# Optimization experiments

Hardware: AMD Instinct MI355X
Metric: run time of the kernel (lower is better)

## Reference

```python
import jax, jax.numpy as jnp
import numpy as np

B, M, NV, H, D = 32, 64, 65, 960, 480
ROUNDS = 5
SCALE = D ** -0.5


def _self_att(x, m, qw, qb):
    # x: [B, P, Q, C] attention over Q within each (b, p); m: [B, P, Q]
    qkv = x @ qw.T + qb                      # [B,P,Q,3C]
    q, k, v = jnp.split(qkv, 3, axis=-1)
    # torch builds mask@mask^T/C from a C-times repeated mask == outer product of mask values
    am = m[..., :, None] * m[..., None, :]   # [B,P,Q,Q]
    a = jnp.einsum('bpqc,bpkc->bpqk', q, k) * SCALE
    a = jnp.where(am == 0, -10000.0, a)
    a = jax.nn.softmax(a, axis=-1)
    return jnp.einsum('bpqk,bpkc->bpqc', a, v)


def _attn_logits(x, mask, qw, qb):
    # Attention_logits.forward: attend over value axis, then over key axis
    x = _self_att(x, mask, qw, qb)
    x = _self_att(jnp.swapaxes(x, 1, 2), jnp.swapaxes(mask, 1, 2), qw, qb)
    return jnp.swapaxes(x, 1, 2)


def _biaffine(x1, x2, W, lw, lb):
    # torch.nn.Bilinear (no bias) on the MxN outer grid + Linear(cat(x1,x2)) with bias,
    # computed without materializing the repeated [B,M,N,2D] tensor.
    d = x1.shape[-1]
    bil = jnp.einsum('bmi,oij,bnj->bmno', x1, W, x2)
    lin = (x1 @ lw[:, :d].T)[:, :, None, :] + (x2 @ lw[:, d:].T)[:, None, :, :] + lb
    return bil + lin


def _rounds(key, value, km, vm, W, lw, lb, fw, fb, qw, qb):
    # shared structure of type_classifier / single_classifier (rounds=5, max pooling)
    lm = km[:, :, None] * vm[:, None, :]     # [B,M,N]
    logits = None
    for i in range(ROUNDS):
        logits = _biaffine(key, value, W, lw, lb)          # [B,M,N,out]
        if i < ROUNDS - 1:
            logits = logits @ fw.T + fb                    # [B,M,N,D]
            logits = _attn_logits(logits, lm, qw, qb)
            key = key + logits.max(axis=2)                 # max-pool over values
            value = value + logits.max(axis=1)             # max-pool over keys
        else:
            logits = logits * lm[..., None]
    return logits


def setup_inputs() -> dict:
    root = jax.random.key(0)
    ks = list(jax.random.split(root, 40))
    it = iter(ks)
    nrm = lambda sh, s=0.02: (jax.random.normal(next(it), sh, jnp.float32) * s)
    key = jax.random.normal(next(it), (B, M, H), jnp.float32)
    value = jax.random.normal(next(it), (B, NV, H), jnp.float32)
    klen = jax.random.randint(next(it), (B,), 1, M + 1)
    key_mask = (jnp.arange(M)[None, :] < klen[:, None]).astype(jnp.float32)
    vlen = jax.random.randint(next(it), (B,), 1, NV + 1)
    value_mask = (jnp.arange(NV)[None, :] < vlen[:, None]).astype(jnp.float32)
    return dict(
        key=key, value=value, key_mask=key_mask, value_mask=value_mask,
        w_kt=nrm((D, H)), b_kt=nrm((D,)), w_vt=nrm((D, H)), b_vt=nrm((D,)),
        w_km=nrm((D, H)), b_km=nrm((D,)), w_vm=nrm((D, H)), b_vm=nrm((D,)),
        w_ks=nrm((D, H)), b_ks=nrm((D,)), w_vs=nrm((D, H)), b_vs=nrm((D,)),
        bt_W=nrm((3, D, D)), bt_lw=nrm((3, 2 * D)), bt_lb=nrm((3,)),
        bi_W=nrm((2, D, D)), bi_lw=nrm((2, 2 * D)), bi_lb=nrm((2,)),
        w_ffnt=nrm((D, 3)), b_ffnt=nrm((D,)), w_ffn=nrm((D, 2)), b_ffn=nrm((D,)),
        qkvt_w=nrm((3 * D, D)), qkvt_b=nrm((3 * D,)),
        qkv_w=nrm((3 * D, D)), qkv_b=nrm((3 * D,)),
        w_cls=nrm((2, 2 * D)), b_cls=nrm((2,)),
    )


def reference(key, value, key_mask, value_mask,
              w_kt, b_kt, w_vt, b_vt, w_km, b_km, w_vm, b_vm,
              w_ks, b_ks, w_vs, b_vs,
              bt_W, bt_lw, bt_lb, bi_W, bi_lw, bi_lb,
              w_ffnt, b_ffnt, w_ffn, b_ffn,
              qkvt_w, qkvt_b, qkv_w, qkv_b, w_cls, b_cls):
    # --- type classifier ---
    kt = key @ w_kt.T + b_kt
    vt = value @ w_vt.T + b_vt
    type_logits = _rounds(kt, vt, key_mask, value_mask,
                          bt_W, bt_lw, bt_lb, w_ffnt, b_ffnt, qkvt_w, qkvt_b)  # [B,M,NV,3]
    # drop type token from values
    v1 = value[:, 1:, :]
    vm1 = value_mask[:, 1:]
    type_token = jax.nn.softmax(type_logits[:, :, 0], axis=-1)   # [B,M,3]
    key_type = jnp.argmax(type_token, axis=-1)
    type_single = key_type == 1
    # --- multi classifier (masks unused, as in original) ---
    km_f = key @ w_km.T + b_km
    vm_f = v1 @ w_vm.T + b_vm
    multi_logits = ((km_f @ w_cls[:, :D].T)[:, :, None, :]
                    + (vm_f @ w_cls[:, D:].T)[:, None, :, :] + b_cls)  # [B,M,M? -> B,64,64,2]
    # --- single classifier with key mask restricted to single-link keys ---
    km2 = (key_mask.astype(bool) & type_single).astype(key_mask.dtype)
    ks_f = key @ w_ks.T + b_ks
    vs_f = v1 @ w_vs.T + b_vs
    single_logits = _rounds(ks_f, vs_f, km2, vm1,
                            bi_W, bi_lw, bi_lb, w_ffn, b_ffn, qkv_w, qkv_b)  # [B,64,64,2]
    return (type_logits, multi_logits, single_logits)
```

## Files before the change

### kernel.cpp

```cpp
#include <hip/hip_runtime.h>
#include <math.h>

constexpr int NB = 32;
constexpr int NM = 64;
constexpr int NNV = 65;
constexpr int NH = 960;
constexpr int ND = 480;
constexpr float ATT_SCALE = 0.045643546458763842f;

constexpr int OF_Pq = 0;
constexpr int OF_cq = 4320;
constexpr int OF_Q2 = 5760;
constexpr int OF_V2 = OF_Q2 + 2*1440;
constexpr int OF_dq = 10080;
constexpr int OF_dv = OF_dq + 2*480;
constexpr int OF_S  = 11520;
constexpr int OF_u  = 11529;
constexpr int OF_r  = 11532;
constexpr int OF_w  = 11535;
constexpr int FOLD_SZ = 11552;

typedef float f32x4 __attribute__((ext_vector_type(4)));
typedef short s16x8 __attribute__((ext_vector_type(8)));

__device__ __forceinline__ float wave_sum(float v) {
#pragma unroll
  for (int d = 32; d; d >>= 1) v += __shfl_xor(v, d);
  return v;
}

__device__ __forceinline__ void split_bf16(float x, short& hi, short& lo) {
  union { float f; unsigned u; } a; a.f = x;
  unsigned uh = a.u + 0x7fffu + ((a.u >> 16) & 1u);
  hi = (short)(uh >> 16);
  union { unsigned u; float f; } b; b.u = ((unsigned)(unsigned short)hi) << 16;
  union { float f; unsigned u; } c; c.f = x - b.f;
  unsigned ul = c.u + 0x7fffu + ((c.u >> 16) & 1u);
  lo = (short)(ul >> 16);
}

struct ProjCfg {
  const float* X; const float* W; const float* bias; float* C;
  int R; int x0; int rpb; int xbs;
};
struct Proj6 { ProjCfg c[6]; };

constexpr int KP = 40;

__global__ __launch_bounds__(256) void k_projM(Proj6 P, int K)
{
  __shared__ unsigned short As_hi[64][KP], As_lo[64][KP];
  __shared__ unsigned short Bs_hi[48][KP], Bs_lo[48][KP];
  int p = blockIdx.x, total = gridDim.x;
  int q = total >> 3, r = total & 7;
  int xk = p & 7, idx = p >> 3;
  int lgc = (xk < r) ? (xk * (q + 1) + idx) : (r * (q + 1) + (xk - r) * q + idx);
  int mp = lgc / 10, nx = lgc - mp * 10;
  ProjCfg cfg; int my;
  if      (mp < 32)  { cfg = P.c[0]; my = mp; }
  else if (mp < 65)  { cfg = P.c[1]; my = mp - 32; }
  else if (mp < 97)  { cfg = P.c[2]; my = mp - 65; }
  else if (mp < 129) { cfg = P.c[3]; my = mp - 97; }
  else if (mp < 161) { cfg = P.c[4]; my = mp - 129; }
  else               { cfg = P.c[5]; my = mp - 161; }
  const int m0 = my * 64, n0 = nx * 48;
  const int tid = threadIdx.x;
  const int l6 = tid & 63, w = tid >> 6;
  const int lr = tid >> 2, kc = (tid & 3) * 8;
  const float* Arow = nullptr;
  {
    int rr = m0 + lr;
    if (rr < cfg.R) {
      int b = rr / cfg.rpb, r2 = rr - b * cfg.rpb;
      Arow = cfg.X + (size_t)b * cfg.xbs + (size_t)(cfg.x0 + r2) * K;
    }
  }
  const float* Brow = (lr < 48) ? (cfg.W + (size_t)(n0 + lr) * K) : nullptr;
  const int fr = l6 & 15, fk = (l6 >> 4) * 8;
  f32x4 acc0 = {0.f, 0.f, 0.f, 0.f}, acc1 = acc0, acc2 = acc0;
  for (int k0 = 0; k0 < K; k0 += 32) {
    float xs[8] = {0.f, 0.f, 0.f, 0.f, 0.f, 0.f, 0.f, 0.f};
    if (Arow) {
      float4 a0 = *(const float4*)(Arow + k0 + kc);
      float4 a1 = *(const float4*)(Arow + k0 + kc + 4);
      xs[0] = a0.x; xs[1] = a0.y; xs[2] = a0.z; xs[3] = a0.w;
      xs[4] = a1.x; xs[5] = a1.y; xs[6] = a1.z; xs[7] = a1.w;
    }
    s16x8 vh, vl;
#pragma unroll
    for (int e = 0; e < 8; ++e) { short h, lo2; split_bf16(xs[e], h, lo2); vh[e] = h; vl[e] = lo2; }
    *(s16x8*)&As_hi[lr][kc] = vh;
    *(s16x8*)&As_lo[lr][kc] = vl;
    if (Brow) {
      float4 b0 = *(const float4*)(Brow + k0 + kc);
      float4 b1 = *(const float4*)(Brow + k0 + kc + 4);
      float ys[8] = {b0.x, b0.y, b0.z, b0.w, b1.x, b1.y, b1.z, b1.w};
      s16x8 wh, wl;
#pragma unroll
      for (int e = 0; e < 8; ++e) { short h, lo2; split_bf16(ys[e], h, lo2); wh[e] = h; wl[e] = lo2; }
      *(s16x8*)&Bs_hi[lr][kc] = wh;
      *(s16x8*)&Bs_lo[lr][kc] = wl;
    }
    __syncthreads();
    s16x8 ah = *(const s16x8*)&As_hi[16 * w + fr][fk];
    s16x8 al = *(const s16x8*)&As_lo[16 * w + fr][fk];
    {
      s16x8 bh = *(const s16x8*)&Bs_hi[fr][fk];
      s16x8 bl = *(const s16x8*)&Bs_lo[fr][fk];
      acc0 = __builtin_amdgcn_mfma_f32_16x16x32_bf16(ah, bh, acc0, 0, 0, 0);
      acc0 = __builtin_amdgcn_mfma_f32_16x16x32_bf16(ah, bl, acc0, 0, 0, 0);
      acc0 = __builtin_amdgcn_mfma_f32_16x16x32_bf16(al, bh, acc0, 0, 0, 0);
    }
    {
      s16x8 bh = *(const s16x8*)&Bs_hi[16 + fr][fk];
      s16x8 bl = *(const s16x8*)&Bs_lo[16 + fr][fk];
      acc1 = __builtin_amdgcn_mfma_f32_16x16x32_bf16(ah, bh, acc1, 0, 0, 0);
      acc1 = __builtin_amdgcn_mfma_f32_16x16x32_bf16(ah, bl, acc1, 0, 0, 0);
      acc1 = __builtin_amdgcn_mfma_f32_16x16x32_bf16(al, bh, acc1, 0, 0, 0);
    }
    {
      s16x8 bh = *(const s16x8*)&Bs_hi[32 + fr][fk];
      s16x8 bl = *(const s16x8*)&Bs_lo[32 + fr][fk];
      acc2 = __builtin_amdgcn_mfma_f32_16x16x32_bf16(ah, bh, acc2, 0, 0, 0);
      acc2 = __builtin_amdgcn_mfma_f32_16x16x32_bf16(ah, bl, acc2, 0, 0, 0);
      acc2 = __builtin_amdgcn_mfma_f32_16x16x32_bf16(al, bh, acc2, 0, 0, 0);
    }
    __syncthreads();
  }
#pragma unroll
  for (int c = 0; c < 3; ++c) {
    f32x4 av = (c == 0) ? acc0 : (c == 1) ? acc1 : acc2;
    int n = n0 + 16 * c + fr;
    float bv = cfg.bias[n];
#pragma unroll
    for (int g = 0; g < 4; ++g) {
      int rr = m0 + 16 * w + (l6 >> 4) * 4 + g;
      if (rr < cfg.R) cfg.C[(size_t)rr * ND + n] = av[g] + bv;
    }
  }
}

__global__ __launch_bounds__(256) void k_tmpM(
    const float* __restrict__ Key, const float* __restrict__ W,
    float* __restrict__ T, int O)
{
  __shared__ unsigned short As_hi[64][KP], As_lo[64][KP];
  __shared__ unsigned short Bs_hi[48][KP], Bs_lo[48][KP];
  const int n0 = blockIdx.x * 48;
  const int o = blockIdx.y, b = blockIdx.z;
  const int tid = threadIdx.x;
  const int l6 = tid & 63, w = tid >> 6;
  const int lr = tid >> 2, kc = (tid & 3) * 8;
  const float* Arow = Key + (size_t)b * NM * ND + (size_t)lr * ND;
  const float* Wo = W + (size_t)o * ND * ND;
  const int fr = l6 & 15, fk = (l6 >> 4) * 8;
  f32x4 acc0 = {0.f, 0.f, 0.f, 0.f}, acc1 = acc0, acc2 = acc0;
  for (int k0 = 0; k0 < ND; k0 += 32) {
    {
      float4 a0 = *(const float4*)(Arow + k0 + kc);
      float4 a1 = *(const float4*)(Arow + k0 + kc + 4);
      float xs[8] = {a0.x, a0.y, a0.z, a0.w, a1.x, a1.y, a1.z, a1.w};
      s16x8 vh, vl;
#pragma unroll
      for (int e = 0; e < 8; ++e) { short h, lo2; split_bf16(xs[e], h, lo2); vh[e] = h; vl[e] = lo2; }
      *(s16x8*)&As_hi[lr][kc] = vh;
      *(s16x8*)&As_lo[lr][kc] = vl;
    }
    if (lr < 48) {
      s16x8 wh, wl;
#pragma unroll
      for (int e = 0; e < 8; ++e) {
        float x = Wo[(size_t)(k0 + kc + e) * ND + n0 + lr];
        short h, lo2; split_bf16(x, h, lo2); wh[e] = h; wl[e] = lo2;
      }
      *(s16x8*)&Bs_hi[lr][kc] = wh;
      *(s16x8*)&Bs_lo[lr][kc] = wl;
    }
    __syncthreads();
    s16x8 ah = *(const s16x8*)&As_hi[16 * w + fr][fk];
    s16x8 al = *(const s16x8*)&As_lo[16 * w + fr][fk];
    {
      s16x8 bh = *(const s16x8*)&Bs_hi[fr][fk];
      s16x8 bl = *(const s16x8*)&Bs_lo[fr][fk];
      acc0 = __builtin_amdgcn_mfma_f32_16x16x32_bf16(ah, bh, acc0, 0, 0, 0);
      acc0 = __builtin_amdgcn_mfma_f32_16x16x32_bf16(ah, bl, acc0, 0, 0, 0);
      acc0 = __builtin_amdgcn_mfma_f32_16x16x32_bf16(al, bh, acc0, 0, 0, 0);
    }
    {
      s16x8 bh = *(const s16x8*)&Bs_hi[16 + fr][fk];
      s16x8 bl = *(const s16x8*)&Bs_lo[16 + fr][fk];
      acc1 = __builtin_amdgcn_mfma_f32_16x16x32_bf16(ah, bh, acc1, 0, 0, 0);
      acc1 = __builtin_amdgcn_mfma_f32_16x16x32_bf16(ah, bl, acc1, 0, 0, 0);
      acc1 = __builtin_amdgcn_mfma_f32_16x16x32_bf16(al, bh, acc1, 0, 0, 0);
    }
    {
      s16x8 bh = *(const s16x8*)&Bs_hi[32 + fr][fk];
      s16x8 bl = *(const s16x8*)&Bs_lo[32 + fr][fk];
      acc2 = __builtin_amdgcn_mfma_f32_16x16x32_bf16(ah, bh, acc2, 0, 0, 0);
      acc2 = __builtin_amdgcn_mfma_f32_16x16x32_bf16(ah, bl, acc2, 0, 0, 0);
      acc2 = __builtin_amdgcn_mfma_f32_16x16x32_bf16(al, bh, acc2, 0, 0, 0);
    }
    __syncthreads();
  }
  float* C = T + ((size_t)(b * O + o) * NM) * ND;
#pragma unroll
  for (int c = 0; c < 3; ++c) {
    f32x4 av = (c == 0) ? acc0 : (c == 1) ? acc1 : acc2;
    int n = n0 + 16 * c + fr;
#pragma unroll
    for (int g = 0; g < 4; ++g) {
      int rr = 16 * w + (l6 >> 4) * 4 + g;
      C[(size_t)rr * ND + n] = av[g];
    }
  }
}

template <int O, int NVX>
__global__ __launch_bounds__(256) void k_bilatt0(
    const float* __restrict__ T, const float* __restrict__ Val,
    const float* __restrict__ linK, const float* __restrict__ linV,
    const float* __restrict__ lb, const float* __restrict__ F,
    const float* __restrict__ km, const float* __restrict__ vm,
    int vmOff, int vmStride, float* __restrict__ Y1)
{
  __shared__ float Ls[NVX][3];
  __shared__ float STs[NVX][3];
  __shared__ float hs[NVX], gs[NVX], mkj[NVX];
  __shared__ float Pm[NVX][66];
  __shared__ float rmx[NVX][3];
  __shared__ float rsum[NVX][3];
  __shared__ float ry[NVX][3][3];
  __shared__ float lvs[NVX][3];
  const int b = blockIdx.x >> 6, m = blockIdx.x & 63;
  const int tid = threadIdx.x;
  const int lane = tid & 63, w = tid >> 6;

  for (int j = tid; j < NVX; j += 256) {
    mkj[j] = vm[b * vmStride + vmOff + j];
#pragma unroll
    for (int o = 0; o < O; ++o) lvs[j][o] = linV[((size_t)b * NVX + j) * O + o];
  }
  float4 tsr[O][2];
#pragma unroll
  for (int o = 0; o < O; ++o) {
    const float4* trow = (const float4*)(T + (((size_t)b * O + o) * NM + m) * (size_t)ND);
    tsr[o][0] = trow[lane];
    tsr[o][1] = (lane < 56) ? trow[64 + lane] : make_float4(0.f, 0.f, 0.f, 0.f);
  }
  float lk[O];
#pragma unroll
  for (int o = 0; o < O; ++o) lk[o] = linK[((size_t)b * NM + m) * O + o] + lb[o];
  const float gm = km[b * NM + m];
  const bool gz = (gm == 0.f);

  for (int n = w; n < NVX; n += 4) {
    const float4* vrow = (const float4*)(Val + ((size_t)b * NVX + n) * (size_t)ND);
    float4 v0 = vrow[lane];
    float4 v1 = (lane < 56) ? vrow[64 + lane] : make_float4(0.f, 0.f, 0.f, 0.f);
    float a[3] = {0.f, 0.f, 0.f};
#pragma unroll
    for (int o = 0; o < O; ++o) {
      a[o] = v0.x * tsr[o][0].x + v0.y * tsr[o][0].y + v0.z * tsr[o][0].z + v0.w * tsr[o][0].w
           + v1.x * tsr[o][1].x + v1.y * tsr[o][1].y + v1.z * tsr[o][1].z + v1.w * tsr[o][1].w;
    }
#pragma unroll
    for (int o = 0; o < O; ++o) a[o] = wave_sum(a[o]);
    if (lane == 0) {
#pragma unroll
      for (int o = 0; o < O; ++o) Ls[n][o] = a[o] + lk[o] + lvs[n][o];
      if (O == 2) Ls[n][2] = 0.f;
    }
  }
  __syncthreads();
  const float* Sm = F + OF_S;
  const float u0 = F[OF_u], u1 = F[OF_u + 1], u2 = F[OF_u + 2];
  const float r0 = F[OF_r], r1 = F[OF_r + 1], r2 = F[OF_r + 2];
  const float wc = F[OF_w];
  if (tid < NVX) {
    int j = tid;
    float t0 = Ls[j][0], t1 = Ls[j][1], t2 = Ls[j][2];
    STs[j][0] = t0 * Sm[0] + t1 * Sm[3] + t2 * Sm[6];
    STs[j][1] = t0 * Sm[1] + t1 * Sm[4] + t2 * Sm[7];
    STs[j][2] = t0 * Sm[2] + t1 * Sm[5] + t2 * Sm[8];
    hs[j] = t0 * u0 + t1 * u1 + t2 * u2;
    gs[j] = t0 * r0 + t1 * r1 + t2 * r2;
  }
  __syncthreads();
  const bool act = tid < NVX * 3;
  int i = 0, qq = 0, jlo = 0, jhi = 0;
  float st0 = 0, st1 = 0, st2 = 0, hi = 0;
  bool rowz = true;
  if (act) {
    i = tid / 3; qq = tid - i * 3;
    jlo = qq * 22; jhi = (jlo + 22 < NVX) ? jlo + 22 : NVX;
    st0 = STs[i][0]; st1 = STs[i][1]; st2 = STs[i][2]; hi = hs[i];
    rowz = gz || (mkj[i] == 0.f);
    float mx = -3.0e38f;
    for (int j = jlo; j < jhi; ++j) {
      float s = st0 * Ls[j][0] + st1 * Ls[j][1] + hi + gs[j] + wc;
      if (O == 3) s += st2 * Ls[j][2];
      s = (rowz || mkj[j] == 0.f) ? -10000.f : ATT_SCALE * s;
      Pm[i][j] = s;
      mx = fmaxf(mx, s);
    }
    rmx[i][qq] = mx;
  }
  __syncthreads();
  if (act) {
    float mx = fmaxf(fmaxf(rmx[i][0], rmx[i][1]), rmx[i][2]);
    float sum = 0.f, y0 = 0.f, y1 = 0.f, y2 = 0.f;
    for (int j = jlo; j < jhi; ++j) {
      float pp = __expf(Pm[i][j] - mx);
      sum += pp; y0 += pp * Ls[j][0]; y1 += pp * Ls[j][1];
      if (O == 3) y2 += pp * Ls[j][2];
    }
    rsum[i][qq] = sum; ry[i][qq][0] = y0; ry[i][qq][1] = y1; ry[i][qq][2] = y2;
  }
  __syncthreads();
  if (tid < NVX) {
    int ii = tid;
    float sum = rsum[ii][0] + rsum[ii][1] + rsum[ii][2];
    float y0 = ry[ii][0][0] + ry[ii][1][0] + ry[ii][2][0];
    float y1 = ry[ii][0][1] + ry[ii][1][1] + ry[ii][2][1];
    float y2 = ry[ii][0][2] + ry[ii][1][2] + ry[ii][2][2];
    float inv = 1.f / sum;
    size_t ob = (((size_t)b * NM + m) * NVX + ii) * O;
    Y1[ob + 0] = y0 * inv;
    Y1[ob + 1] = y1 * inv;
    if (O == 3) Y1[ob + 2] = y2 * inv;
  }
}

template <int O, int NVX>
__global__ __launch_bounds__(256) void k_att1vupd(
    const float* __restrict__ Y1, float* __restrict__ Y2,
    const float* __restrict__ F,
    const float* __restrict__ km, const float* __restrict__ vm,
    int vmOff, int vmStride,
    float* __restrict__ valb, const float* __restrict__ lw,
    float* __restrict__ linV)
{
  __shared__ float Ys1[NM][3];
  __shared__ float STs[NM][3];
  __shared__ float hs[NM], gs[NM], mkm[NM];
  __shared__ float Pm[NM][66];
  __shared__ float rmx[NM][3];
  __shared__ float rsum[NM][3];
  __shared__ float ry[NM][3][3];
  __shared__ float Ys2[NM][3];
  __shared__ float vrow[ND];
  const int b = blockIdx.x / NVX, n = blockIdx.x - b * NVX;
  const int tid = threadIdx.x;
  for (int u = tid; u < NM * O; u += 256) {
    int mm = u % NM, o = u / NM;
    Ys1[mm][o] = Y1[(((size_t)b * NM + mm) * NVX + n) * O + o];
  }
  if (tid < NM) {
    mkm[tid] = km[b * NM + tid];
    if (O == 2) Ys1[tid][2] = 0.f;
  }
  const float gm = vm[b * vmStride + vmOff + n];
  const bool gz = (gm == 0.f);
  __syncthreads();
  const float* Sm = F + OF_S + 16;
  const float u0 = F[OF_u + 16], u1 = F[OF_u + 17], u2 = F[OF_u + 18];
  const float r0 = F[OF_r + 16], r1 = F[OF_r + 17], r2 = F[OF_r + 18];
  const float wc = F[OF_w + 16];
  if (tid < NM) {
    int j = tid;
    float t0 = Ys1[j][0], t1 = Ys1[j][1], t2 = Ys1[j][2];
    STs[j][0] = t0 * Sm[0] + t1 * Sm[3] + t2 * Sm[6];
    STs[j][1] = t0 * Sm[1] + t1 * Sm[4] + t2 * Sm[7];
    STs[j][2] = t0 * Sm[2] + t1 * Sm[5] + t2 * Sm[8];
    hs[j] = t0 * u0 + t1 * u1 + t2 * u2;
    gs[j] = t0 * r0 + t1 * r1 + t2 * r2;
  }
  __syncthreads();
  const bool act = tid < NM * 3;
  int i = 0, qq = 0, jlo = 0, jhi = 0;
  float st0 = 0, st1 = 0, st2 = 0, hi = 0;
  bool rowz = true;
  if (act) {
    i = tid / 3; qq = tid - i * 3;
    jlo = qq * 22; jhi = (jlo + 22 < NM) ? jlo + 22 : NM;
    st0 = STs[i][0]; st1 = STs[i][1]; st2 = STs[i][2]; hi = hs[i];
    rowz = gz || (mkm[i] == 0.f);
    float mx = -3.0e38f;
    for (int j = jlo; j < jhi; ++j) {
      float s = st0 * Ys1[j][0] + st1 * Ys1[j][1] + hi + gs[j] + wc;
      if (O == 3) s += st2 * Ys1[j][2];
      s = (rowz || mkm[j] == 0.f) ? -10000.f : ATT_SCALE * s;
      Pm[i][j] = s;
      mx = fmaxf(mx, s);
    }
    rmx[i][qq] = mx;
  }
  __syncthreads();
  if (act) {
    float mx = fmaxf(fmaxf(rmx[i][0], rmx[i][1]), rmx[i][2]);
    float sum = 0.f, y0 = 0.f, y1 = 0.f, y2 = 0.f;
    for (int j = jlo; j < jhi; ++j) {
      float pp = __expf(Pm[i][j] - mx);
      sum += pp; y0 += pp * Ys1[j][0]; y1 += pp * Ys1[j][1];
      if (O == 3) y2 += pp * Ys1[j][2];
    }
    rsum[i][qq] = sum; ry[i][qq][0] = y0; ry[i][qq][1] = y1; ry[i][qq][2] = y2;
  }
  __syncthreads();
  if (tid < NM) {
    int ii = tid;
    float sum = rsum[ii][0] + rsum[ii][1] + rsum[ii][2];
    float y0 = ry[ii][0][0] + ry[ii][1][0] + ry[ii][2][0];
    float y1 = ry[ii][0][1] + ry[ii][1][1] + ry[ii][2][1];
    float y2 = ry[ii][0][2] + ry[ii][1][2] + ry[ii][2][2];
    float inv = 1.f / sum;
    y0 *= inv; y1 *= inv; y2 *= inv;
    size_t ob = (((size_t)b * NVX + n) * NM + ii) * O;
    Y2[ob + 0] = y0; Y2[ob + 1] = y1;
    if (O == 3) Y2[ob + 2] = y2;
    Ys2[ii][0] = y0; Ys2[ii][1] = y1; Ys2[ii][2] = (O == 3) ? y2 : 0.f;
  }
  __syncthreads();
  const float* V2 = F + OF_V2;
  const float* dv = F + OF_dv;
  for (int d = tid; d < ND; d += 256) {
    float v0 = V2[d], v1 = V2[ND + d], v2 = (O == 3) ? V2[2 * ND + d] : 0.f;
    float mx = -3.0e38f;
    for (int j = 0; j < NM; ++j) {
      float s = Ys2[j][0] * v0 + Ys2[j][1] * v1;
      if (O == 3) s += Ys2[j][2] * v2;
      mx = fmaxf(mx, s);
    }
    size_t di = ((size_t)b * NVX + n) * ND + d;
    float nv = valb[di] + mx + dv[d];
    valb[di] = nv;
    vrow[d] = nv;
  }
  __syncthreads();
  const int wv = tid >> 6, lane = tid & 63;
  if (wv < O) {
    float acc = 0.f;
    for (int d = lane; d < ND; d += 64) acc += vrow[d] * lw[(size_t)wv * 2 * ND + ND + d];
    acc = wave_sum(acc);
    if (lane == 0) linV[((size_t)b * NVX + n) * O + wv] = acc;
  }
}

template <int O, int NVX>
__global__ __launch_bounds__(256) void k_kupd(
    const float* __restrict__ Y2, const float* __restrict__ F,
    float* __restrict__ keyb, const float* __restrict__ lw,
    float* __restrict__ linK)
{
  __shared__ float Ys[NVX][3];
  __shared__ float krow[ND];
  const int b = blockIdx.x >> 6, m = blockIdx.x & 63;
  const int tid = threadIdx.x;
  for (int u = tid; u < NVX * O; u += 256) {
    int j = u % NVX, o = u / NVX;
    Ys[j][o] = Y2[(((size_t)b * NVX + j) * NM + m) * O + o];
  }
  __syncthreads();
  const float* V2 = F + OF_V2;
  const float* dv = F + OF_dv;
  for (int d = tid; d < ND; d += 256) {
    float v0 = V2[d], v1 = V2[ND + d], v2 = (O == 3) ? V2[2 * ND + d] : 0.f;
    float mx = -3.0e38f;
    for (int j = 0; j < NVX; ++j) {
      float s = Ys[j][0] * v0 + Ys[j][1] * v1;
      if (O == 3) s += Ys[j][2] * v2;
      mx = fmaxf(mx, s);
    }
    size_t di = ((size_t)b * NM + m) * ND + d;
    float nv = keyb[di] + mx + dv[d];
    keyb[di] = nv;
    krow[d] = nv;
  }
  __syncthreads();
  const int wv = tid >> 6, lane = tid & 63;
  if (wv < O) {
    float acc = 0.f;
    for (int d = lane; d < ND; d += 64) acc += krow[d] * lw[(size_t)wv * 2 * ND + d];
    acc = wave_sum(acc);
    if (lane == 0) linK[((size_t)b * NM + m) * O + wv] = acc;
  }
}

template <int O, int NVX>
__global__ __launch_bounds__(256) void k_bilfin(
    const float* __restrict__ T, const float* __restrict__ Val,
    const float* __restrict__ linK, const float* __restrict__ linV,
    const float* __restrict__ lb, const float* __restrict__ km,
    const float* __restrict__ vm, int vmOff, int vmStride,
    float* __restrict__ Out)
{
  const int b = blockIdx.x >> 6, m = blockIdx.x & 63;
  const int tid = threadIdx.x;
  const int lane = tid & 63, w = tid >> 6;
  float4 tsr[O][2];
#pragma unroll
  for (int o = 0; o < O; ++o) {
    const float4* trow = (const float4*)(T + (((size_t)b * O + o) * NM + m) * (size_t)ND);
    tsr[o][0] = trow[lane];
    tsr[o][1] = (lane < 56) ? trow[64 + lane] : make_float4(0.f, 0.f, 0.f, 0.f);
  }
  float lk[O];
#pragma unroll
  for (int o = 0; o < O; ++o) lk[o] = linK[((size_t)b * NM + m) * O + o] + lb[o];
  const float kmv = km[b * NM + m];
  for (int n = w; n < NVX; n += 4) {
    const float4* vrow = (const float4*)(Val + ((size_t)b * NVX + n) * (size_t)ND);
    float4 v0 = vrow[lane];
    float4 v1 = (lane < 56) ? vrow[64 + lane] : make_float4(0.f, 0.f, 0.f, 0.f);
    float a[3] = {0.f, 0.f, 0.f};
#pragma unroll
    for (int o = 0; o < O; ++o) {
      a[o] = v0.x * tsr[o][0].x + v0.y * tsr[o][0].y + v0.z * tsr[o][0].z + v0.w * tsr[o][0].w
           + v1.x * tsr[o][1].x + v1.y * tsr[o][1].y + v1.z * tsr[o][1].z + v1.w * tsr[o][1].w;
    }
#pragma unroll
    for (int o = 0; o < O; ++o) a[o] = wave_sum(a[o]);
    if (lane == 0) {
      float msk = kmv * vm[b * vmStride + vmOff + n];
      size_t ob = (((size_t)b * NM + m) * NVX + n) * O;
#pragma unroll
      for (int o = 0; o < O; ++o)
        Out[ob + o] = (a[o] + lk[o] + linV[((size_t)b * NVX + n) * O + o]) * msk;
    }
  }
}

struct SpCfg { const float* X; const float* W; float* Out; int R; int O; int wStride; int wOff; };
__global__ __launch_bounds__(256) void k_sproj6(
    SpCfg s0, SpCfg s1, SpCfg s2, SpCfg s3, SpCfg s4, SpCfg s5)
{
  int z = blockIdx.y;
  SpCfg c = (z == 0) ? s0 : (z == 1) ? s1 : (z == 2) ? s2 : (z == 3) ? s3 : (z == 4) ? s4 : s5;
  int gid = blockIdx.x * 4 + (threadIdx.x >> 6);
  if (gid >= c.R * c.O) return;
  int lane = threadIdx.x & 63;
  int r = gid / c.O, o = gid - r * c.O;
  const float* x = c.X + (size_t)r * ND;
  const float* wp = c.W + (size_t)o * c.wStride + c.wOff;
  float acc = 0.f;
  for (int d = lane; d < ND; d += 64) acc += x[d] * wp[d];
  acc = wave_sum(acc);
  if (lane == 0) c.Out[gid] = acc;
}

struct FoldCfg { const float* fw; const float* fb; const float* qw; const float* qb; float* F; int O; };

__global__ __launch_bounds__(256) void k_fold1B(FoldCfg A, FoldCfg Bc)
{
  FoldCfg c = (blockIdx.y == 0) ? A : Bc;
  int O = c.O;
  int gid = blockIdx.x * 4 + (threadIdx.x >> 6);
  int lane = threadIdx.x & 63;
  if (gid >= 3 * ND) return;
  int part = gid / ND, cc0 = gid - part * ND;
  const float* qrow = c.qw + (size_t)(part * ND + cc0) * ND;
  float p0 = 0.f, p1 = 0.f, p2 = 0.f, cc = 0.f;
  for (int d = lane; d < ND; d += 64) {
    float q = qrow[d];
    p0 += c.fw[d * O + 0] * q;
    p1 += c.fw[d * O + 1] * q;
    if (O == 3) p2 += c.fw[d * O + 2] * q;
    cc += c.fb[d] * q;
  }
  p0 = wave_sum(p0); p1 = wave_sum(p1); p2 = wave_sum(p2); cc = wave_sum(cc);
  if (lane == 0) {
    c.F[OF_Pq + part * 1440 + 0 * ND + cc0] = p0;
    c.F[OF_Pq + part * 1440 + 1 * ND + cc0] = p1;
    c.F[OF_Pq + part * 1440 + 2 * ND + cc0] = (O == 3) ? p2 : 0.f;
    c.F[OF_cq + part * ND + cc0] = cc + c.qb[part * ND + cc0];
  }
}

__global__ __launch_bounds__(256) void k_fold2B(FoldCfg A, FoldCfg Bc)
{
  FoldCfg c = (blockIdx.y == 0) ? A : Bc;
  int O = c.O;
  float* F = c.F;
  int gid = blockIdx.x * 4 + (threadIdx.x >> 6);
  int lane = threadIdx.x & 63;
  if (gid < 3 * ND) {
    int part = gid / ND, cc0 = gid - part * ND;
    const float* qrow = c.qw + (size_t)(part * ND + cc0) * ND;
    const float* Pv = F + OF_Pq + 2 * 1440;
    const float* cv = F + OF_cq + 2 * ND;
    float p0 = 0.f, p1 = 0.f, p2 = 0.f, cc = 0.f;
    for (int d = lane; d < ND; d += 64) {
      float q = qrow[d];
      p0 += Pv[0 * ND + d] * q;
      p1 += Pv[1 * ND + d] * q;
      if (O == 3) p2 += Pv[2 * ND + d] * q;
      cc += cv[d] * q;
    }
    p0 = wave_sum(p0); p1 = wave_sum(p1); p2 = wave_sum(p2); cc = wave_sum(cc);
    if (lane == 0) {
      F[OF_Q2 + part * 1440 + 0 * ND + cc0] = p0;
      F[OF_Q2 + part * 1440 + 1 * ND + cc0] = p1;
      F[OF_Q2 + part * 1440 + 2 * ND + cc0] = (O == 3) ? p2 : 0.f;
      F[OF_dq + part * ND + cc0] = cc + c.qb[part * ND + cc0];
    }
  } else if (gid < 3 * ND + 16) {
    int s = gid - 3 * ND;
    const float* Pq = F + OF_Pq;
    const float* Pk = F + OF_Pq + 1440;
    const float* cq = F + OF_cq;
    const float* ck = F + OF_cq + ND;
    float acc = 0.f;
    if (s < 9) {
      int o = s / 3, op = s % 3;
      bool ok = (o < O) && (op < O);
      if (ok) for (int q = lane; q < ND; q += 64) acc += Pq[o * ND + q] * Pk[op * ND + q];
      acc = wave_sum(acc);
      if (lane == 0) F[OF_S + s] = ok ? acc : 0.f;
    } else if (s < 12) {
      int o = s - 9; bool ok = o < O;
      if (ok) for (int q = lane; q < ND; q += 64) acc += Pq[o * ND + q] * ck[q];
      acc = wave_sum(acc);
      if (lane == 0) F[OF_u + o] = ok ? acc : 0.f;
    } else if (s < 15) {
      int o = s - 12; bool ok = o < O;
      if (ok) for (int q = lane; q < ND; q += 64) acc += cq[q] * Pk[o * ND + q];
      acc = wave_sum(acc);
      if (lane == 0) F[OF_r + o] = ok ? acc : 0.f;
    } else {
      for (int q = lane; q < ND; q += 64) acc += cq[q] * ck[q];
      acc = wave_sum(acc);
      if (lane == 0) F[OF_w] = acc;
    }
  }
}

__global__ __launch_bounds__(256) void k_fold3B(FoldCfg A, FoldCfg Bc)
{
  FoldCfg c = (blockIdx.y == 0) ? A : Bc;
  int O = c.O;
  float* F = c.F;
  int s = blockIdx.x * 4 + (threadIdx.x >> 6);
  int lane = threadIdx.x & 63;
  if (s >= 16) return;
  const float* Q2 = F + OF_Q2;
  const float* K2 = F + OF_Q2 + 1440;
  const float* dq = F + OF_dq;
  const float* dk = F + OF_dq + ND;
  float acc = 0.f;
  if (s < 9) {
    int o = s / 3, op = s % 3;
    bool ok = (o < O) && (op < O);
    if (ok) for (int q = lane; q < ND; q += 64) acc += Q2[o * ND + q] * K2[op * ND + q];
    acc = wave_sum(acc);
    if (lane == 0) F[OF_S + 16 + s] = ok ? acc : 0.f;
  } else if (s < 12) {
    int o = s - 9; bool ok = o < O;
    if (ok) for (int q = lane; q < ND; q += 64) acc += Q2[o * ND + q] * dk[q];
    acc = wave_sum(acc);
    if (lane == 0) F[OF_u + 16 + o] = ok ? acc : 0.f;
  } else if (s < 15) {
    int o = s - 12; bool ok = o < O;
    if (ok) for (int q = lane; q < ND; q += 64) acc += dq[q] * K2[o * ND + q];
    acc = wave_sum(acc);
    if (lane == 0) F[OF_r + 16 + o] = ok ? acc : 0.f;
  } else {
    for (int q = lane; q < ND; q += 64) acc += dq[q] * dk[q];
    acc = wave_sum(acc);
    if (lane == 0) F[OF_w + 16] = acc;
  }
}

__global__ void k_type(const float* __restrict__ tl, const float* __restrict__ key_mask,
                       float* __restrict__ km2)
{
  int i = blockIdx.x * blockDim.x + threadIdx.x;
  if (i >= NB * NM) return;
  const float* p = tl + (size_t)i * NNV * 3;
  float l0 = p[0], l1 = p[1], l2 = p[2];
  int arg = 0;
  float best = l0;
  if (l1 > best) { best = l1; arg = 1; }
  if (l2 > best) { best = l2; arg = 2; }
  km2[i] = (key_mask[i] != 0.f && arg == 1) ? 1.f : 0.f;
}

__global__ void k_multi(const float* __restrict__ a, const float* __restrict__ bb,
                        const float* __restrict__ bc, float* __restrict__ out)
{
  int i = blockIdx.x * blockDim.x + threadIdx.x;
  if (i >= NB * NM * NM * 2) return;
  int c = i & 1;
  int t = i >> 1;
  int n = t % NM; t /= NM;
  int m = t % NM;
  int b = t / NM;
  out[i] = a[((size_t)b * NM + m) * 2 + c] + bb[((size_t)b * NM + n) * 2 + c] + bc[c];
}

template <int O, int NVX>
static void run_rounds(hipStream_t stream,
                       float* keyb, float* valb,
                       const float* kmp, const float* vmp, int vmOff, int vmStride,
                       const float* Wb, const float* lwp, const float* lbp,
                       float* fold, float* linK, float* linV,
                       float* tmp, float* Y1, float* Y2, float* outp)
{
  dim3 blk(256);
  for (int r = 0; r < 5; ++r) {
    k_tmpM<<<dim3(10, O, NB), blk, 0, stream>>>(keyb, Wb, tmp, O);
    if (r < 4) {
      k_bilatt0<O, NVX><<<dim3(NB * NM), blk, 0, stream>>>(
          tmp, valb, linK, linV, lbp, fold, kmp, vmp, vmOff, vmStride, Y1);
      k_att1vupd<O, NVX><<<dim3(NB * NVX), blk, 0, stream>>>(
          Y1, Y2, fold, kmp, vmp, vmOff, vmStride, valb, lwp, linV);
      k_kupd<O, NVX><<<dim3(NB * NM), blk, 0, stream>>>(Y2, fold, keyb, lwp, linK);
    } else {
      k_bilfin<O, NVX><<<dim3(NB * NM), blk, 0, stream>>>(
          tmp, valb, linK, linV, lbp, kmp, vmp, vmOff, vmStride, outp);
    }
  }
}

extern "C" void kernel_launch(void* const* d_in, const int* in_sizes, int n_in,
                              void* d_out, int out_size, void* d_ws, size_t ws_size,
                              hipStream_t stream)
{
  const float* key        = (const float*)d_in[0];
  const float* value      = (const float*)d_in[1];
  const float* key_mask   = (const float*)d_in[2];
  const float* value_mask = (const float*)d_in[3];
  const float* w_kt = (const float*)d_in[4];  const float* b_kt = (const float*)d_in[5];
  const float* w_vt = (const float*)d_in[6];  const float* b_vt = (const float*)d_in[7];
  const float* w_km = (const float*)d_in[8];  const float* b_km = (const float*)d_in[9];
  const float* w_vm = (const float*)d_in[10]; const float* b_vm = (const float*)d_in[11];
  const float* w_ks = (const float*)d_in[12]; const float* b_ks = (const float*)d_in[13];
  const float* w_vs = (const float*)d_in[14]; const float* b_vs = (const float*)d_in[15];
  const float* bt_W = (const float*)d_in[16]; const float* bt_lw = (const float*)d_in[17];
  const float* bt_lb = (const float*)d_in[18];
  const float* bi_W = (const float*)d_in[19]; const float* bi_lw = (const float*)d_in[20];
  const float* bi_lb = (const float*)d_in[21];
  const float* w_ffnt = (const float*)d_in[22]; const float* b_ffnt = (const float*)d_in[23];
  const float* w_ffn  = (const float*)d_in[24]; const float* b_ffn  = (const float*)d_in[25];
  const float* qkvt_w = (const float*)d_in[26]; const float* qkvt_b = (const float*)d_in[27];
  const float* qkv_w  = (const float*)d_in[28]; const float* qkv_b  = (const float*)d_in[29];
  const float* w_cls  = (const float*)d_in[30]; const float* b_cls  = (const float*)d_in[31];

  float* ws = (float*)d_ws;
  size_t off = 0;
  float* kt_t  = ws + off; off += (size_t)NB * NM * ND;
  float* vt_t  = ws + off; off += (size_t)NB * NNV * ND;
  float* kt_s  = ws + off; off += (size_t)NB * NM * ND;
  float* vt_s  = ws + off; off += (size_t)NB * NM * ND;
  float* tmp   = ws + off; off += (size_t)NB * 3 * NM * ND;
  float* Y1    = ws + off; off += (size_t)NB * NM * NNV * 3;
  float* Y2    = ws + off; off += (size_t)NB * NM * NNV * 3;
  float* linK_t = ws + off; off += (size_t)NB * NM * 3;
  float* linV_t = ws + off; off += (size_t)NB * NNV * 3;
  float* linK_s = ws + off; off += (size_t)NB * NM * 3;
  float* linV_s = ws + off; off += (size_t)NB * NM * 3;
  float* fold_t = ws + off; off += FOLD_SZ;
  float* fold_s = ws + off; off += FOLD_SZ;
  float* km2   = ws + off; off += (size_t)NB * NM;
  float* a2    = ws + off; off += (size_t)NB * NM * 2;
  float* b2    = ws + off; off += (size_t)NB * NM * 2;
  (void)off; (void)ws_size; (void)in_sizes; (void)n_in; (void)out_size;

  float* kmf = tmp;
  float* vmf = tmp + (size_t)NB * NM * ND;

  float* out_type   = (float*)d_out;
  float* out_multi  = out_type + (size_t)NB * NM * NNV * 3;
  float* out_single = out_multi + (size_t)NB * NM * NM * 2;

  dim3 blk(256);

  Proj6 P;
  P.c[0] = { key,   w_kt, b_kt, kt_t, NB * NM,  0, NM,  NM * NH };
  P.c[1] = { value, w_vt, b_vt, vt_t, NB * NNV, 0, NNV, NNV * NH };
  P.c[2] = { key,   w_ks, b_ks, kt_s, NB * NM,  0, NM,  NM * NH };
  P.c[3] = { value, w_vs, b_vs, vt_s, NB * NM,  1, NM,  NNV * NH };
  P.c[4] = { key,   w_km, b_km, kmf,  NB * NM,  0, NM,  NM * NH };
  P.c[5] = { value, w_vm, b_vm, vmf,  NB * NM,  1, NM,  NNV * NH };
  k_projM<<<dim3(193 * 10), blk, 0, stream>>>(P, NH);

  FoldCfg ft = { w_ffnt, b_ffnt, qkvt_w, qkvt_b, fold_t, 3 };
  FoldCfg fs = { w_ffn,  b_ffn,  qkv_w,  qkv_b,  fold_s, 2 };
  k_fold1B<<<dim3(360, 2), blk, 0, stream>>>(ft, fs);
  k_fold2B<<<dim3(364, 2), blk, 0, stream>>>(ft, fs);
  k_fold3B<<<dim3(4, 2), blk, 0, stream>>>(ft, fs);

  SpCfg s0 = { kt_t, bt_lw, linK_t, NB * NM,  3, 2 * ND, 0 };
  SpCfg s1 = { vt_t, bt_lw, linV_t, NB * NNV, 3, 2 * ND, ND };
  SpCfg s2 = { kt_s, bi_lw, linK_s, NB * NM,  2, 2 * ND, 0 };
  SpCfg s3 = { vt_s, bi_lw, linV_s, NB * NM,  2, 2 * ND, ND };
  SpCfg s4 = { kmf,  w_cls, a2,     NB * NM,  2, 2 * ND, 0 };
  SpCfg s5 = { vmf,  w_cls, b2,     NB * NM,  2, 2 * ND, ND };
  k_sproj6<<<dim3((NB * NNV * 3 + 3) / 4, 6), blk, 0, stream>>>(s0, s1, s2, s3, s4, s5);

  k_multi<<<dim3((NB * NM * NM * 2 + 255) / 256), blk, 0, stream>>>(a2, b2, b_cls, out_multi);

  run_rounds<3, NNV>(stream, kt_t, vt_t, key_mask, value_mask, 0, NNV,
                     bt_W, bt_lw, bt_lb, fold_t, linK_t, linV_t,
                     tmp, Y1, Y2, out_type);

  k_type<<<dim3(8), blk, 0, stream>>>(out_type, key_mask, km2);

  run_rounds<2, NM>(stream, kt_s, vt_s, km2, value_mask, 1, NNV,
                    bi_W, bi_lw, bi_lb, fold_s, linK_s, linV_s,
                    tmp, Y1, Y2, out_single);
}
```

Before: 1.097 ms.

## Fuse all biaffine-attention rounds into one persistent per-batch mega kernel

Replaces the per-round sequence of bilinear, attention and key/value update kernels with a single 1024-thread kernel per batch that loops over all five rounds. Bilinear weights are pre-transposed and split into bf16 hi/lo once, and key/value states are kept as bf16 hi/lo pairs updated in place, with logits held in shared memory. This removes dozens of launches and global round-trips of intermediate tensors. The cost is only 32 blocks across the GPU, leaving most compute units idle.

```diff
diff --git a/kernel.cpp b/kernel.cpp
--- a/kernel.cpp
+++ b/kernel.cpp
@@ -20,6 +20,7 @@
 constexpr int OF_w  = 11535;
 constexpr int FOLD_SZ = 11552;
 
+typedef unsigned short u16;
 typedef float f32x4 __attribute__((ext_vector_type(4)));
 typedef short s16x8 __attribute__((ext_vector_type(8)));
 
@@ -39,8 +40,39 @@
   lo = (short)(ul >> 16);
 }
 
+__device__ __forceinline__ float join_bf16(u16 h, u16 l) {
+  union { unsigned u; float f; } a, b;
+  a.u = ((unsigned)h) << 16; b.u = ((unsigned)l) << 16;
+  return a.f + b.f;
+}
+
+__global__ __launch_bounds__(256) void k_cvtT(
+    const float* __restrict__ btW, const float* __restrict__ biW,
+    u16* __restrict__ wtHi, u16* __restrict__ wtLo)
+{
+  __shared__ float s[32][33];
+  const int z = blockIdx.z;
+  const float* src = (z < 3) ? (btW + (size_t)z * ND * ND) : (biW + (size_t)(z - 3) * ND * ND);
+  u16* dh = wtHi + (size_t)z * ND * ND;
+  u16* dl = wtLo + (size_t)z * ND * ND;
+  const int k0 = blockIdx.y * 32, n0 = blockIdx.x * 32;
+  const int tx = threadIdx.x & 31, ty = threadIdx.x >> 5;
+#pragma unroll
+  for (int q = 0; q < 4; ++q)
+    s[ty + q * 8][tx] = src[(size_t)(k0 + ty + q * 8) * ND + n0 + tx];
+  __syncthreads();
+#pragma unroll
+  for (int q = 0; q < 4; ++q) {
+    float v = s[tx][ty + q * 8];
+    short h, l; split_bf16(v, h, l);
+    size_t di = (size_t)(n0 + ty + q * 8) * ND + k0 + tx;
+    dh[di] = (u16)h; dl[di] = (u16)l;
+  }
+}
+
 struct ProjCfg {
   const float* X; const float* W; const float* bias; float* C;
+  u16* pH; u16* pL;
   int R; int x0; int rpb; int xbs;
 };
 struct Proj6 { ProjCfg c[6]; };
@@ -49,8 +81,8 @@
 
 __global__ __launch_bounds__(256) void k_projM(Proj6 P, int K)
 {
-  __shared__ unsigned short As_hi[64][KP], As_lo[64][KP];
-  __shared__ unsigned short Bs_hi[48][KP], Bs_lo[48][KP];
+  __shared__ u16 As_hi[64][KP], As_lo[64][KP];
+  __shared__ u16 Bs_hi[48][KP], Bs_lo[48][KP];
   int p = blockIdx.x, total = gridDim.x;
   int q = total >> 3, r = total & 7;
   int xk = p & 7, idx = p >> 3;
@@ -135,397 +167,263 @@
 #pragma unroll
     for (int g = 0; g < 4; ++g) {
       int rr = m0 + 16 * w + (l6 >> 4) * 4 + g;
-      if (rr < cfg.R) cfg.C[(size_t)rr * ND + n] = av[g] + bv;
-    }
-  }
-}
-
-__global__ __launch_bounds__(256) void k_tmpM(
-    const float* __restrict__ Key, const float* __restrict__ W,
-    float* __restrict__ T, int O)
-{
-  __shared__ unsigned short As_hi[64][KP], As_lo[64][KP];
-  __shared__ unsigned short Bs_hi[48][KP], Bs_lo[48][KP];
-  const int n0 = blockIdx.x * 48;
-  const int o = blockIdx.y, b = blockIdx.z;
+      if (rr < cfg.R) {
+        float v = av[g] + bv;
+        size_t di = (size_t)rr * ND + n;
+        cfg.C[di] = v;
+        if (cfg.pH) {
+          short h, lo2; split_bf16(v, h, lo2);
+          cfg.pH[di] = (u16)h; cfg.pL[di] = (u16)lo2;
+        }
+      }
+    }
+  }
+}
+
+template <int O, int NVX>
+__global__ __launch_bounds__(1024, 4) void k_mega(
+    const u16* __restrict__ WtH, const u16* __restrict__ WtL,
+    u16* __restrict__ tmpH, u16* __restrict__ tmpL,
+    u16* __restrict__ keyH, u16* __restrict__ keyL,
+    u16* __restrict__ valH, u16* __restrict__ valL,
+    const float* __restrict__ kmp, const float* __restrict__ vmp, int vmOff, int vmStride,
+    const float* __restrict__ F, const float* __restrict__ lw, const float* __restrict__ lb,
+    const float* __restrict__ linK0, const float* __restrict__ linV0,
+    float* __restrict__ outp)
+{
+  constexpr int NT = (NVX + 15) >> 4;
+  __shared__ float Lb[NM][NVX][3];
+  __shared__ float Yb[NM][NVX][3];
+  __shared__ float linKL[NM][3];
+  __shared__ float linVL[NVX][3];
+  __shared__ float kmL[NM];
+  __shared__ float vmL[NVX];
+  const int b = blockIdx.x;
   const int tid = threadIdx.x;
-  const int l6 = tid & 63, w = tid >> 6;
-  const int lr = tid >> 2, kc = (tid & 3) * 8;
-  const float* Arow = Key + (size_t)b * NM * ND + (size_t)lr * ND;
-  const float* Wo = W + (size_t)o * ND * ND;
-  const int fr = l6 & 15, fk = (l6 >> 4) * 8;
-  f32x4 acc0 = {0.f, 0.f, 0.f, 0.f}, acc1 = acc0, acc2 = acc0;
-  for (int k0 = 0; k0 < ND; k0 += 32) {
+  const int w = tid >> 6, l = tid & 63;
+  const int fr = l & 15, fko = (l >> 4) * 8;
+  const int rquad = (l >> 4) * 4;
+
+  if (tid < NM) {
+    kmL[tid] = kmp[b * NM + tid];
+#pragma unroll
+    for (int o = 0; o < O; ++o) linKL[tid][o] = linK0[(size_t)(b * NM + tid) * O + o];
+  } else if (tid >= 128 && tid - 128 < NVX) {
+    int n = tid - 128;
+    vmL[n] = vmp[b * vmStride + vmOff + n];
+#pragma unroll
+    for (int o = 0; o < O; ++o) linVL[n][o] = linV0[(size_t)(b * NVX + n) * O + o];
+  }
+  float SmA[9], SmB[9];
+#pragma unroll
+  for (int s = 0; s < 9; ++s) { SmA[s] = F[OF_S + s]; SmB[s] = F[OF_S + 16 + s]; }
+  float uA[3], uB[3], rA[3], rB[3];
+#pragma unroll
+  for (int s = 0; s < 3; ++s) {
+    uA[s] = F[OF_u + s]; uB[s] = F[OF_u + 16 + s];
+    rA[s] = F[OF_r + s]; rB[s] = F[OF_r + 16 + s];
+  }
+  const float wA = F[OF_w], wB = F[OF_w + 16];
+  const float* V2 = F + OF_V2;
+  const float* dvp = F + OF_dv;
+
+  const size_t bK = (size_t)b * NM * ND;
+  const size_t bV = (size_t)b * NVX * ND;
+  u16* tH = tmpH + (size_t)b * O * NM * ND;
+  u16* tL = tmpL + (size_t)b * O * NM * ND;
+  const u16* kHb = keyH + bK; const u16* kLb = keyL + bK;
+  const u16* vHb = valH + bV; const u16* vLb = valL + bV;
+  const s16x8 zf = {0, 0, 0, 0, 0, 0, 0, 0};
+
+  for (int r = 0; r < 5; ++r) {
+    __syncthreads();
     {
-      float4 a0 = *(const float4*)(Arow + k0 + kc);
-      float4 a1 = *(const float4*)(Arow + k0 + kc + 4);
-      float xs[8] = {a0.x, a0.y, a0.z, a0.w, a1.x, a1.y, a1.z, a1.w};
-      s16x8 vh, vl;
-#pragma unroll
-      for (int e = 0; e < 8; ++e) { short h, lo2; split_bf16(xs[e], h, lo2); vh[e] = h; vl[e] = lo2; }
-      *(s16x8*)&As_hi[lr][kc] = vh;
-      *(s16x8*)&As_lo[lr][kc] = vl;
-    }
-    if (lr < 48) {
-      s16x8 wh, wl;
-#pragma unroll
-      for (int e = 0; e < 8; ++e) {
-        float x = Wo[(size_t)(k0 + kc + e) * ND + n0 + lr];
-        short h, lo2; split_bf16(x, h, lo2); wh[e] = h; wl[e] = lo2;
+      const int GJ = O * 30;
+      for (int t = w; t < GJ; t += 16) {
+        int o = t / 30, nt = t - o * 30;
+        const u16* bH = WtH + ((size_t)o * ND + nt * 16 + fr) * ND + fko;
+        const u16* bL2 = WtL + ((size_t)o * ND + nt * 16 + fr) * ND + fko;
+        f32x4 z4 = {0.f, 0.f, 0.f, 0.f};
+        f32x4 am[4] = {z4, z4, z4, z4};
+#pragma unroll 3
+        for (int k0 = 0; k0 < ND; k0 += 32) {
+          s16x8 bh = *(const s16x8*)(bH + k0);
+          s16x8 bl = *(const s16x8*)(bL2 + k0);
+#pragma unroll
+          for (int mt = 0; mt < 4; ++mt) {
+            s16x8 ah = *(const s16x8*)(kHb + (size_t)(mt * 16 + fr) * ND + fko + k0);
+            s16x8 al = *(const s16x8*)(kLb + (size_t)(mt * 16 + fr) * ND + fko + k0);
+            am[mt] = __builtin_amdgcn_mfma_f32_16x16x32_bf16(ah, bh, am[mt], 0, 0, 0);
+            am[mt] = __builtin_amdgcn_mfma_f32_16x16x32_bf16(ah, bl, am[mt], 0, 0, 0);
+            am[mt] = __builtin_amdgcn_mfma_f32_16x16x32_bf16(al, bh, am[mt], 0, 0, 0);
+          }
+        }
+        int n = nt * 16 + fr;
+#pragma unroll
+        for (int mt = 0; mt < 4; ++mt)
+#pragma unroll
+          for (int g = 0; g < 4; ++g) {
+            int m = mt * 16 + rquad + g;
+            short h, lo2; split_bf16(am[mt][g], h, lo2);
+            size_t di = ((size_t)o * NM + m) * ND + n;
+            tH[di] = (u16)h; tL[di] = (u16)lo2;
+          }
       }
-      *(s16x8*)&Bs_hi[lr][kc] = wh;
-      *(s16x8*)&Bs_lo[lr][kc] = wl;
     }
     __syncthreads();
-    s16x8 ah = *(const s16x8*)&As_hi[16 * w + fr][fk];
-    s16x8 al = *(const s16x8*)&As_lo[16 * w + fr][fk];
+    const bool finalr = (r == 4);
     {
-      s16x8 bh = *(const s16x8*)&Bs_hi[fr][fk];
-      s16x8 bl = *(const s16x8*)&Bs_lo[fr][fk];
-      acc0 = __builtin_amdgcn_mfma_f32_16x16x32_bf16(ah, bh, acc0, 0, 0, 0);
-      acc0 = __builtin_amdgcn_mfma_f32_16x16x32_bf16(ah, bl, acc0, 0, 0, 0);
-      acc0 = __builtin_amdgcn_mfma_f32_16x16x32_bf16(al, bh, acc0, 0, 0, 0);
-    }
-    {
-      s16x8 bh = *(const s16x8*)&Bs_hi[16 + fr][fk];
-      s16x8 bl = *(const s16x8*)&Bs_lo[16 + fr][fk];
-      acc1 = __builtin_amdgcn_mfma_f32_16x16x32_bf16(ah, bh, acc1, 0, 0, 0);
-      acc1 = __builtin_amdgcn_mfma_f32_16x16x32_bf16(ah, bl, acc1, 0, 0, 0);
-      acc1 = __builtin_amdgcn_mfma_f32_16x16x32_bf16(al, bh, acc1, 0, 0, 0);
-    }
-    {
-      s16x8 bh = *(const s16x8*)&Bs_hi[32 + fr][fk];
-      s16x8 bl = *(const s16x8*)&Bs_lo[32 + fr][fk];
-      acc2 = __builtin_amdgcn_mfma_f32_16x16x32_bf16(ah, bh, acc2, 0, 0, 0);
-      acc2 = __builtin_amdgcn_mfma_f32_16x16x32_bf16(ah, bl, acc2, 0, 0, 0);
-      acc2 = __builtin_amdgcn_mfma_f32_16x16x32_bf16(al, bh, acc2, 0, 0, 0);
-    }
+      const int BJ = O * NT;
+      for (int t = w; t < BJ; t += 16) {
+        int o = t / NT, nt = t - o * NT;
+        int n = nt * 16 + fr;
+        bool nok = n < NVX;
+        const u16* bH = vHb + (size_t)(nok ? n : 0) * ND + fko;
+        const u16* bL2 = vLb + (size_t)(nok ? n : 0) * ND + fko;
+        f32x4 z4 = {0.f, 0.f, 0.f, 0.f};
+        f32x4 am[4] = {z4, z4, z4, z4};
+#pragma unroll 3
+        for (int k0 = 0; k0 < ND; k0 += 32) {
+          s16x8 bh = nok ? *(const s16x8*)(bH + k0) : zf;
+          s16x8 bl = nok ? *(const s16x8*)(bL2 + k0) : zf;
+#pragma unroll
+          for (int mt = 0; mt < 4; ++mt) {
+            s16x8 ah = *(const s16x8*)(tH + ((size_t)o * NM + mt * 16 + fr) * ND + fko + k0);
+            s16x8 al = *(const s16x8*)(tL + ((size_t)o * NM + mt * 16 + fr) * ND + fko + k0);
+            am[mt] = __builtin_amdgcn_mfma_f32_16x16x32_bf16(ah, bh, am[mt], 0, 0, 0);
+            am[mt] = __builtin_amdgcn_mfma_f32_16x16x32_bf16(ah, bl, am[mt], 0, 0, 0);
+            am[mt] = __builtin_amdgcn_mfma_f32_16x16x32_bf16(al, bh, am[mt], 0, 0, 0);
+          }
+        }
+        if (nok) {
+          float lbo = lb[o];
+#pragma unroll
+          for (int mt = 0; mt < 4; ++mt)
+#pragma unroll
+            for (int g = 0; g < 4; ++g) {
+              int m = mt * 16 + rquad + g;
+              float v = am[mt][g] + linKL[m][o] + linVL[n][o] + lbo;
+              if (!finalr) Lb[m][n][o] = v;
+              else outp[(((size_t)b * NM + m) * NVX + n) * O + o] = v * kmL[m] * vmL[n];
+            }
+        }
+      }
+    }
+    if (finalr) break;
     __syncthreads();
-  }
-  float* C = T + ((size_t)(b * O + o) * NM) * ND;
-#pragma unroll
-  for (int c = 0; c < 3; ++c) {
-    f32x4 av = (c == 0) ? acc0 : (c == 1) ? acc1 : acc2;
-    int n = n0 + 16 * c + fr;
-#pragma unroll
-    for (int g = 0; g < 4; ++g) {
-      int rr = 16 * w + (l6 >> 4) * 4 + g;
-      C[(size_t)rr * ND + n] = av[g];
-    }
-  }
-}
-
-template <int O, int NVX>
-__global__ __launch_bounds__(256) void k_bilatt0(
-    const float* __restrict__ T, const float* __restrict__ Val,
-    const float* __restrict__ linK, const float* __restrict__ linV,
-    const float* __restrict__ lb, const float* __restrict__ F,
-    const float* __restrict__ km, const float* __restrict__ vm,
-    int vmOff, int vmStride, float* __restrict__ Y1)
-{
-  __shared__ float Ls[NVX][3];
-  __shared__ float STs[NVX][3];
-  __shared__ float hs[NVX], gs[NVX], mkj[NVX];
-  __shared__ float Pm[NVX][66];
-  __shared__ float rmx[NVX][3];
-  __shared__ float rsum[NVX][3];
-  __shared__ float ry[NVX][3][3];
-  __shared__ float lvs[NVX][3];
-  const int b = blockIdx.x >> 6, m = blockIdx.x & 63;
-  const int tid = threadIdx.x;
-  const int lane = tid & 63, w = tid >> 6;
-
-  for (int j = tid; j < NVX; j += 256) {
-    mkj[j] = vm[b * vmStride + vmOff + j];
-#pragma unroll
-    for (int o = 0; o < O; ++o) lvs[j][o] = linV[((size_t)b * NVX + j) * O + o];
-  }
-  float4 tsr[O][2];
-#pragma unroll
-  for (int o = 0; o < O; ++o) {
-    const float4* trow = (const float4*)(T + (((size_t)b * O + o) * NM + m) * (size_t)ND);
-    tsr[o][0] = trow[lane];
-    tsr[o][1] = (lane < 56) ? trow[64 + lane] : make_float4(0.f, 0.f, 0.f, 0.f);
-  }
-  float lk[O];
-#pragma unroll
-  for (int o = 0; o < O; ++o) lk[o] = linK[((size_t)b * NM + m) * O + o] + lb[o];
-  const float gm = km[b * NM + m];
-  const bool gz = (gm == 0.f);
-
-  for (int n = w; n < NVX; n += 4) {
-    const float4* vrow = (const float4*)(Val + ((size_t)b * NVX + n) * (size_t)ND);
-    float4 v0 = vrow[lane];
-    float4 v1 = (lane < 56) ? vrow[64 + lane] : make_float4(0.f, 0.f, 0.f, 0.f);
-    float a[3] = {0.f, 0.f, 0.f};
-#pragma unroll
-    for (int o = 0; o < O; ++o) {
-      a[o] = v0.x * tsr[o][0].x + v0.y * tsr[o][0].y + v0.z * tsr[o][0].z + v0.w * tsr[o][0].w
-           + v1.x * tsr[o][1].x + v1.y * tsr[o][1].y + v1.z * tsr[o][1].z + v1.w * tsr[o][1].w;
-    }
-#pragma unroll
-    for (int o = 0; o < O; ++o) a[o] = wave_sum(a[o]);
-    if (lane == 0) {
-#pragma unroll
-      for (int o = 0; o < O; ++o) Ls[n][o] = a[o] + lk[o] + lvs[n][o];
-      if (O == 2) Ls[n][2] = 0.f;
-    }
-  }
-  __syncthreads();
-  const float* Sm = F + OF_S;
-  const float u0 = F[OF_u], u1 = F[OF_u + 1], u2 = F[OF_u + 2];
-  const float r0 = F[OF_r], r1 = F[OF_r + 1], r2 = F[OF_r + 2];
-  const float wc = F[OF_w];
-  if (tid < NVX) {
-    int j = tid;
-    float t0 = Ls[j][0], t1 = Ls[j][1], t2 = Ls[j][2];
-    STs[j][0] = t0 * Sm[0] + t1 * Sm[3] + t2 * Sm[6];
-    STs[j][1] = t0 * Sm[1] + t1 * Sm[4] + t2 * Sm[7];
-    STs[j][2] = t0 * Sm[2] + t1 * Sm[5] + t2 * Sm[8];
-    hs[j] = t0 * u0 + t1 * u1 + t2 * u2;
-    gs[j] = t0 * r0 + t1 * r1 + t2 * r2;
-  }
-  __syncthreads();
-  const bool act = tid < NVX * 3;
-  int i = 0, qq = 0, jlo = 0, jhi = 0;
-  float st0 = 0, st1 = 0, st2 = 0, hi = 0;
-  bool rowz = true;
-  if (act) {
-    i = tid / 3; qq = tid - i * 3;
-    jlo = qq * 22; jhi = (jlo + 22 < NVX) ? jlo + 22 : NVX;
-    st0 = STs[i][0]; st1 = STs[i][1]; st2 = STs[i][2]; hi = hs[i];
-    rowz = gz || (mkj[i] == 0.f);
-    float mx = -3.0e38f;
-    for (int j = jlo; j < jhi; ++j) {
-      float s = st0 * Ls[j][0] + st1 * Ls[j][1] + hi + gs[j] + wc;
-      if (O == 3) s += st2 * Ls[j][2];
-      s = (rowz || mkj[j] == 0.f) ? -10000.f : ATT_SCALE * s;
-      Pm[i][j] = s;
-      mx = fmaxf(mx, s);
-    }
-    rmx[i][qq] = mx;
-  }
-  __syncthreads();
-  if (act) {
-    float mx = fmaxf(fmaxf(rmx[i][0], rmx[i][1]), rmx[i][2]);
-    float sum = 0.f, y0 = 0.f, y1 = 0.f, y2 = 0.f;
-    for (int j = jlo; j < jhi; ++j) {
-      float pp = __expf(Pm[i][j] - mx);
-      sum += pp; y0 += pp * Ls[j][0]; y1 += pp * Ls[j][1];
-      if (O == 3) y2 += pp * Ls[j][2];
-    }
-    rsum[i][qq] = sum; ry[i][qq][0] = y0; ry[i][qq][1] = y1; ry[i][qq][2] = y2;
-  }
-  __syncthreads();
-  if (tid < NVX) {
-    int ii = tid;
-    float sum = rsum[ii][0] + rsum[ii][1] + rsum[ii][2];
-    float y0 = ry[ii][0][0] + ry[ii][1][0] + ry[ii][2][0];
-    float y1 = ry[ii][0][1] + ry[ii][1][1] + ry[ii][2][1];
-    float y2 = ry[ii][0][2] + ry[ii][1][2] + ry[ii][2][2];
-    float inv = 1.f / sum;
-    size_t ob = (((size_t)b * NM + m) * NVX + ii) * O;
-    Y1[ob + 0] = y0 * inv;
-    Y1[ob + 1] = y1 * inv;
-    if (O == 3) Y1[ob + 2] = y2 * inv;
-  }
-}
-
-template <int O, int NVX>
-__global__ __launch_bounds__(256) void k_att1vupd(
-    const float* __restrict__ Y1, float* __restrict__ Y2,
-    const float* __restrict__ F,
-    const float* __restrict__ km, const float* __restrict__ vm,
-    int vmOff, int vmStride,
-    float* __restrict__ valb, const float* __restrict__ lw,
-    float* __restrict__ linV)
-{
-  __shared__ float Ys1[NM][3];
-  __shared__ float STs[NM][3];
-  __shared__ float hs[NM], gs[NM], mkm[NM];
-  __shared__ float Pm[NM][66];
-  __shared__ float rmx[NM][3];
-  __shared__ float rsum[NM][3];
-  __shared__ float ry[NM][3][3];
-  __shared__ float Ys2[NM][3];
-  __shared__ float vrow[ND];
-  const int b = blockIdx.x / NVX, n = blockIdx.x - b * NVX;
-  const int tid = threadIdx.x;
-  for (int u = tid; u < NM * O; u += 256) {
-    int mm = u % NM, o = u / NM;
-    Ys1[mm][o] = Y1[(((size_t)b * NM + mm) * NVX + n) * O + o];
-  }
-  if (tid < NM) {
-    mkm[tid] = km[b * NM + tid];
-    if (O == 2) Ys1[tid][2] = 0.f;
-  }
-  const float gm = vm[b * vmStride + vmOff + n];
-  const bool gz = (gm == 0.f);
-  __syncthreads();
-  const float* Sm = F + OF_S + 16;
-  const float u0 = F[OF_u + 16], u1 = F[OF_u + 17], u2 = F[OF_u + 18];
-  const float r0 = F[OF_r + 16], r1 = F[OF_r + 17], r2 = F[OF_r + 18];
-  const float wc = F[OF_w + 16];
-  if (tid < NM) {
-    int j = tid;
-    float t0 = Ys1[j][0], t1 = Ys1[j][1], t2 = Ys1[j][2];
-    STs[j][0] = t0 * Sm[0] + t1 * Sm[3] + t2 * Sm[6];
-    STs[j][1] = t0 * Sm[1] + t1 * Sm[4] + t2 * Sm[7];
-    STs[j][2] = t0 * Sm[2] + t1 * Sm[5] + t2 * Sm[8];
-    hs[j] = t0 * u0 + t1 * u1 + t2 * u2;
-    gs[j] = t0 * r0 + t1 * r1 + t2 * r2;
-  }
-  __syncthreads();
-  const bool act = tid < NM * 3;
-  int i = 0, qq = 0, jlo = 0, jhi = 0;
-  float st0 = 0, st1 = 0, st2 = 0, hi = 0;
-  bool rowz = true;
-  if (act) {
-    i = tid / 3; qq = tid - i * 3;
-    jlo = qq * 22; jhi = (jlo + 22 < NM) ? jlo + 22 : NM;
-    st0 = STs[i][0]; st1 = STs[i][1]; st2 = STs[i][2]; hi = hs[i];
-    rowz = gz || (mkm[i] == 0.f);
-    float mx = -3.0e38f;
-    for (int j = jlo; j < jhi; ++j) {
-      float s = st0 * Ys1[j][0] + st1 * Ys1[j][1] + hi + gs[j] + wc;
-      if (O == 3) s += st2 * Ys1[j][2];
-      s = (rowz || mkm[j] == 0.f) ? -10000.f : ATT_SCALE * s;
-      Pm[i][j] = s;
-      mx = fmaxf(mx, s);
-    }
-    rmx[i][qq] = mx;
-  }
-  __syncthreads();
-  if (act) {
-    float mx = fmaxf(fmaxf(rmx[i][0], rmx[i][1]), rmx[i][2]);
-    float sum = 0.f, y0 = 0.f, y1 = 0.f, y2 = 0.f;
-    for (int j = jlo; j < jhi; ++j) {
-      float pp = __expf(Pm[i][j] - mx);
-      sum += pp; y0 += pp * Ys1[j][0]; y1 += pp * Ys1[j][1];
-      if (O == 3) y2 += pp * Ys1[j][2];
-    }
-    rsum[i][qq] = sum; ry[i][qq][0] = y0; ry[i][qq][1] = y1; ry[i][qq][2] = y2;
-  }
-  __syncthreads();
-  if (tid < NM) {
-    int ii = tid;
-    float sum = rsum[ii][0] + rsum[ii][1] + rsum[ii][2];
-    float y0 = ry[ii][0][0] + ry[ii][1][0] + ry[ii][2][0];
-    float y1 = ry[ii][0][1] + ry[ii][1][1] + ry[ii][2][1];
-    float y2 = ry[ii][0][2] + ry[ii][1][2] + ry[ii][2][2];
-    float inv = 1.f / sum;
-    y0 *= inv; y1 *= inv; y2 *= inv;
-    size_t ob = (((size_t)b * NVX + n) * NM + ii) * O;
-    Y2[ob + 0] = y0; Y2[ob + 1] = y1;
-    if (O == 3) Y2[ob + 2] = y2;
-    Ys2[ii][0] = y0; Ys2[ii][1] = y1; Ys2[ii][2] = (O == 3) ? y2 : 0.f;
-  }
-  __syncthreads();
-  const float* V2 = F + OF_V2;
-  const float* dv = F + OF_dv;
-  for (int d = tid; d < ND; d += 256) {
-    float v0 = V2[d], v1 = V2[ND + d], v2 = (O == 3) ? V2[2 * ND + d] : 0.f;
-    float mx = -3.0e38f;
-    for (int j = 0; j < NM; ++j) {
-      float s = Ys2[j][0] * v0 + Ys2[j][1] * v1;
-      if (O == 3) s += Ys2[j][2] * v2;
-      mx = fmaxf(mx, s);
-    }
-    size_t di = ((size_t)b * NVX + n) * ND + d;
-    float nv = valb[di] + mx + dv[d];
-    valb[di] = nv;
-    vrow[d] = nv;
-  }
-  __syncthreads();
-  const int wv = tid >> 6, lane = tid & 63;
-  if (wv < O) {
-    float acc = 0.f;
-    for (int d = lane; d < ND; d += 64) acc += vrow[d] * lw[(size_t)wv * 2 * ND + ND + d];
-    acc = wave_sum(acc);
-    if (lane == 0) linV[((size_t)b * NVX + n) * O + wv] = acc;
-  }
-}
-
-template <int O, int NVX>
-__global__ __launch_bounds__(256) void k_kupd(
-    const float* __restrict__ Y2, const float* __restrict__ F,
-    float* __restrict__ keyb, const float* __restrict__ lw,
-    float* __restrict__ linK)
-{
-  __shared__ float Ys[NVX][3];
-  __shared__ float krow[ND];
-  const int b = blockIdx.x >> 6, m = blockIdx.x & 63;
-  const int tid = threadIdx.x;
-  for (int u = tid; u < NVX * O; u += 256) {
-    int j = u % NVX, o = u / NVX;
-    Ys[j][o] = Y2[(((size_t)b * NVX + j) * NM + m) * O + o];
-  }
-  __syncthreads();
-  const float* V2 = F + OF_V2;
-  const float* dv = F + OF_dv;
-  for (int d = tid; d < ND; d += 256) {
-    float v0 = V2[d], v1 = V2[ND + d], v2 = (O == 3) ? V2[2 * ND + d] : 0.f;
-    float mx = -3.0e38f;
-    for (int j = 0; j < NVX; ++j) {
-      float s = Ys[j][0] * v0 + Ys[j][1] * v1;
-      if (O == 3) s += Ys[j][2] * v2;
-      mx = fmaxf(mx, s);
-    }
-    size_t di = ((size_t)b * NM + m) * ND + d;
-    float nv = keyb[di] + mx + dv[d];
-    keyb[di] = nv;
-    krow[d] = nv;
-  }
-  __syncthreads();
-  const int wv = tid >> 6, lane = tid & 63;
-  if (wv < O) {
-    float acc = 0.f;
-    for (int d = lane; d < ND; d += 64) acc += krow[d] * lw[(size_t)wv * 2 * ND + d];
-    acc = wave_sum(acc);
-    if (lane == 0) linK[((size_t)b * NM + m) * O + wv] = acc;
-  }
-}
-
-template <int O, int NVX>
-__global__ __launch_bounds__(256) void k_bilfin(
-    const float* __restrict__ T, const float* __restrict__ Val,
-    const float* __restrict__ linK, const float* __restrict__ linV,
-    const float* __restrict__ lb, const float* __restrict__ km,
-    const float* __restrict__ vm, int vmOff, int vmStride,
-    float* __restrict__ Out)
-{
-  const int b = blockIdx.x >> 6, m = blockIdx.x & 63;
-  const int tid = threadIdx.x;
-  const int lane = tid & 63, w = tid >> 6;
-  float4 tsr[O][2];
-#pragma unroll
-  for (int o = 0; o < O; ++o) {
-    const float4* trow = (const float4*)(T + (((size_t)b * O + o) * NM + m) * (size_t)ND);
-    tsr[o][0] = trow[lane];
-    tsr[o][1] = (lane < 56) ? trow[64 + lane] : make_float4(0.f, 0.f, 0.f, 0.f);
-  }
-  float lk[O];
-#pragma unroll
-  for (int o = 0; o < O; ++o) lk[o] = linK[((size_t)b * NM + m) * O + o] + lb[o];
-  const float kmv = km[b * NM + m];
-  for (int n = w; n < NVX; n += 4) {
-    const float4* vrow = (const float4*)(Val + ((size_t)b * NVX + n) * (size_t)ND);
-    float4 v0 = vrow[lane];
-    float4 v1 = (lane < 56) ? vrow[64 + lane] : make_float4(0.f, 0.f, 0.f, 0.f);
-    float a[3] = {0.f, 0.f, 0.f};
-#pragma unroll
-    for (int o = 0; o < O; ++o) {
-      a[o] = v0.x * tsr[o][0].x + v0.y * tsr[o][0].y + v0.z * tsr[o][0].z + v0.w * tsr[o][0].w
-           + v1.x * tsr[o][1].x + v1.y * tsr[o][1].y + v1.z * tsr[o][1].z + v1.w * tsr[o][1].w;
-    }
-#pragma unroll
-    for (int o = 0; o < O; ++o) a[o] = wave_sum(a[o]);
-    if (lane == 0) {
-      float msk = kmv * vm[b * vmStride + vmOff + n];
-      size_t ob = (((size_t)b * NM + m) * NVX + n) * O;
-#pragma unroll
-      for (int o = 0; o < O; ++o)
-        Out[ob + o] = (a[o] + lk[o] + linV[((size_t)b * NVX + n) * O + o]) * msk;
+    for (int job = tid; job < NM * NVX; job += 1024) {
+      int m = job / NVX, i = job - m * NVX;
+      float Li0 = Lb[m][i][0], Li1 = Lb[m][i][1], Li2 = (O == 3) ? Lb[m][i][2] : 0.f;
+      float st0 = Li0 * SmA[0] + Li1 * SmA[3] + Li2 * SmA[6];
+      float st1 = Li0 * SmA[1] + Li1 * SmA[4] + Li2 * SmA[7];
+      float st2 = Li0 * SmA[2] + Li1 * SmA[5] + Li2 * SmA[8];
+      float hi = Li0 * uA[0] + Li1 * uA[1] + Li2 * uA[2];
+      bool rowz = (kmL[m] == 0.f) || (vmL[i] == 0.f);
+      float mx = -3.0e38f, sum = 0.f, y0 = 0.f, y1 = 0.f, y2 = 0.f;
+      for (int j = 0; j < NVX; ++j) {
+        float t0 = Lb[m][j][0], t1 = Lb[m][j][1], t2 = (O == 3) ? Lb[m][j][2] : 0.f;
+        float s = st0 * t0 + st1 * t1 + st2 * t2 + hi
+                + (t0 * rA[0] + t1 * rA[1] + t2 * rA[2]) + wA;
+        s = (rowz || vmL[j] == 0.f) ? -10000.f : ATT_SCALE * s;
+        float nm = fmaxf(mx, s);
+        float p = __expf(s - nm), cc = __expf(mx - nm);
+        sum = sum * cc + p; y0 = y0 * cc + p * t0; y1 = y1 * cc + p * t1; y2 = y2 * cc + p * t2;
+        mx = nm;
+      }
+      float inv = 1.f / sum;
+      Yb[m][i][0] = y0 * inv; Yb[m][i][1] = y1 * inv;
+      if (O == 3) Yb[m][i][2] = y2 * inv;
+    }
+    __syncthreads();
+    for (int job = tid; job < NVX * NM; job += 1024) {
+      int n = job / NM, i = job - n * NM;
+      float Yi0 = Yb[i][n][0], Yi1 = Yb[i][n][1], Yi2 = (O == 3) ? Yb[i][n][2] : 0.f;
+      float st0 = Yi0 * SmB[0] + Yi1 * SmB[3] + Yi2 * SmB[6];
+      float st1 = Yi0 * SmB[1] + Yi1 * SmB[4] + Yi2 * SmB[7];
+      float st2 = Yi0 * SmB[2] + Yi1 * SmB[5] + Yi2 * SmB[8];
+      float hi = Yi0 * uB[0] + Yi1 * uB[1] + Yi2 * uB[2];
+      bool rowz = (vmL[n] == 0.f) || (kmL[i] == 0.f);
+      float mx = -3.0e38f, sum = 0.f, y0 = 0.f, y1 = 0.f, y2 = 0.f;
+      for (int j = 0; j < NM; ++j) {
+        float t0 = Yb[j][n][0], t1 = Yb[j][n][1], t2 = (O == 3) ? Yb[j][n][2] : 0.f;
+        float s = st0 * t0 + st1 * t1 + st2 * t2 + hi
+                + (t0 * rB[0] + t1 * rB[1] + t2 * rB[2]) + wB;
+        s = (rowz || kmL[j] == 0.f) ? -10000.f : ATT_SCALE * s;
+        float nm = fmaxf(mx, s);
+        float p = __expf(s - nm), cc = __expf(mx - nm);
+        sum = sum * cc + p; y0 = y0 * cc + p * t0; y1 = y1 * cc + p * t1; y2 = y2 * cc + p * t2;
+        mx = nm;
+      }
+      float inv = 1.f / sum;
+      Lb[i][n][0] = y0 * inv; Lb[i][n][1] = y1 * inv;
+      if (O == 3) Lb[i][n][2] = y2 * inv;
+    }
+    __syncthreads();
+    for (int u = tid; u < (NVX + NM) * 120; u += 1024) {
+      if (u < NVX * 120) {
+        int n = u / 120, dg = u - n * 120; int d0 = dg * 4;
+        float v0[4], v1[4], v2[4], dl4[4];
+#pragma unroll
+        for (int e = 0; e < 4; ++e) {
+          v0[e] = V2[d0 + e]; v1[e] = V2[ND + d0 + e];
+          v2[e] = (O == 3) ? V2[2 * ND + d0 + e] : 0.f;
+          dl4[e] = dvp[d0 + e];
+        }
+        float mx[4] = {-3.0e38f, -3.0e38f, -3.0e38f, -3.0e38f};
+        for (int j = 0; j < NM; ++j) {
+          float y0 = Lb[j][n][0], y1 = Lb[j][n][1], y2 = (O == 3) ? Lb[j][n][2] : 0.f;
+#pragma unroll
+          for (int e = 0; e < 4; ++e)
+            mx[e] = fmaxf(mx[e], y0 * v0[e] + y1 * v1[e] + y2 * v2[e]);
+        }
+        float p0 = 0.f, p1 = 0.f, p2 = 0.f;
+#pragma unroll
+        for (int e = 0; e < 4; ++e) {
+          float delta = mx[e] + dl4[e];
+          size_t gi = bV + (size_t)n * ND + d0 + e;
+          float nv = join_bf16(valH[gi], valL[gi]) + delta;
+          short h, lo2; split_bf16(nv, h, lo2);
+          valH[gi] = (u16)h; valL[gi] = (u16)lo2;
+          p0 += delta * lw[ND + d0 + e];
+          p1 += delta * lw[2 * ND + ND + d0 + e];
+          if (O == 3) p2 += delta * lw[4 * ND + ND + d0 + e];
+        }
+        atomicAdd(&linVL[n][0], p0);
+        atomicAdd(&linVL[n][1], p1);
+        if (O == 3) atomicAdd(&linVL[n][2], p2);
+      } else {
+        int u2 = u - NVX * 120;
+        int m = u2 / 120, dg = u2 - m * 120; int d0 = dg * 4;
+        float v0[4], v1[4], v2[4], dl4[4];
+#pragma unroll
+        for (int e = 0; e < 4; ++e) {
+          v0[e] = V2[d0 + e]; v1[e] = V2[ND + d0 + e];
+          v2[e] = (O == 3) ? V2[2 * ND + d0 + e] : 0.f;
+          dl4[e] = dvp[d0 + e];
+        }
+        float mx[4] = {-3.0e38f, -3.0e38f, -3.0e38f, -3.0e38f};
+        for (int j = 0; j < NVX; ++j) {
+          float y0 = Lb[m][j][0], y1 = Lb[m][j][1], y2 = (O == 3) ? Lb[m][j][2] : 0.f;
+#pragma unroll
+          for (int e = 0; e < 4; ++e)
+            mx[e] = fmaxf(mx[e], y0 * v0[e] + y1 * v1[e] + y2 * v2[e]);
+        }
+        float p0 = 0.f, p1 = 0.f, p2 = 0.f;
+#pragma unroll
+        for (int e = 0; e < 4; ++e) {
+          float delta = mx[e] + dl4[e];
+          size_t gi = bK + (size_t)m * ND + d0 + e;
+          float nv = join_bf16(keyH[gi], keyL[gi]) + delta;
+          short h, lo2; split_bf16(nv, h, lo2);
+          keyH[gi] = (u16)h; keyL[gi] = (u16)lo2;
+          p0 += delta * lw[d0 + e];
+          p1 += delta * lw[2 * ND + d0 + e];
+          if (O == 3) p2 += delta * lw[4 * ND + d0 + e];
+        }
+        atomicAdd(&linKL[m][0], p0);
+        atomicAdd(&linKL[m][1], p1);
+        if (O == 3) atomicAdd(&linKL[m][2], p2);
+      }
     }
   }
 }
@@ -697,30 +595,6 @@
   out[i] = a[((size_t)b * NM + m) * 2 + c] + bb[((size_t)b * NM + n) * 2 + c] + bc[c];
 }
 
-template <int O, int NVX>
-static void run_rounds(hipStream_t stream,
-                       float* keyb, float* valb,
-                       const float* kmp, const float* vmp, int vmOff, int vmStride,
-                       const float* Wb, const float* lwp, const float* lbp,
-                       float* fold, float* linK, float* linV,
-                       float* tmp, float* Y1, float* Y2, float* outp)
-{
-  dim3 blk(256);
-  for (int r = 0; r < 5; ++r) {
-    k_tmpM<<<dim3(10, O, NB), blk, 0, stream>>>(keyb, Wb, tmp, O);
-    if (r < 4) {
-      k_bilatt0<O, NVX><<<dim3(NB * NM), blk, 0, stream>>>(
-          tmp, valb, linK, linV, lbp, fold, kmp, vmp, vmOff, vmStride, Y1);
-      k_att1vupd<O, NVX><<<dim3(NB * NVX), blk, 0, stream>>>(
-          Y1, Y2, fold, kmp, vmp, vmOff, vmStride, valb, lwp, linV);
-      k_kupd<O, NVX><<<dim3(NB * NM), blk, 0, stream>>>(Y2, fold, keyb, lwp, linK);
-    } else {
-      k_bilfin<O, NVX><<<dim3(NB * NM), blk, 0, stream>>>(
-          tmp, valb, linK, linV, lbp, kmp, vmp, vmOff, vmStride, outp);
-    }
-  }
-}
-
 extern "C" void kernel_launch(void* const* d_in, const int* in_sizes, int n_in,
                               void* d_out, int out_size, void* d_ws, size_t ws_size,
                               hipStream_t stream)
@@ -747,26 +621,37 @@
 
   float* ws = (float*)d_ws;
   size_t off = 0;
-  float* kt_t  = ws + off; off += (size_t)NB * NM * ND;
-  float* vt_t  = ws + off; off += (size_t)NB * NNV * ND;
-  float* kt_s  = ws + off; off += (size_t)NB * NM * ND;
-  float* vt_s  = ws + off; off += (size_t)NB * NM * ND;
-  float* tmp   = ws + off; off += (size_t)NB * 3 * NM * ND;
-  float* Y1    = ws + off; off += (size_t)NB * NM * NNV * 3;
-  float* Y2    = ws + off; off += (size_t)NB * NM * NNV * 3;
-  float* linK_t = ws + off; off += (size_t)NB * NM * 3;
-  float* linV_t = ws + off; off += (size_t)NB * NNV * 3;
-  float* linK_s = ws + off; off += (size_t)NB * NM * 3;
-  float* linV_s = ws + off; off += (size_t)NB * NM * 3;
-  float* fold_t = ws + off; off += FOLD_SZ;
-  float* fold_s = ws + off; off += FOLD_SZ;
-  float* km2   = ws + off; off += (size_t)NB * NM;
-  float* a2    = ws + off; off += (size_t)NB * NM * 2;
-  float* b2    = ws + off; off += (size_t)NB * NM * 2;
-  (void)off; (void)ws_size; (void)in_sizes; (void)n_in; (void)out_size;
-
-  float* kmf = tmp;
-  float* vmf = tmp + (size_t)NB * NM * ND;
+  auto alloc = [&](size_t nfloat) { float* p = ws + off; off += (nfloat + 3) & ~(size_t)3; return p; };
+
+  float* kt_t = alloc((size_t)NB * NM * ND);
+  float* vt_t = alloc((size_t)NB * NNV * ND);
+  float* kt_s = alloc((size_t)NB * NM * ND);
+  float* vt_s = alloc((size_t)NB * NM * ND);
+  float* kmf  = alloc((size_t)NB * NM * ND);
+  float* vmf  = alloc((size_t)NB * NM * ND);
+  float* linK_t = alloc((size_t)NB * NM * 3);
+  float* linV_t = alloc((size_t)NB * NNV * 3);
+  float* linK_s = alloc((size_t)NB * NM * 2);
+  float* linV_s = alloc((size_t)NB * NM * 2);
+  float* fold_t = alloc(FOLD_SZ);
+  float* fold_s = alloc(FOLD_SZ);
+  float* km2 = alloc((size_t)NB * NM);
+  float* a2  = alloc((size_t)NB * NM * 2);
+  float* b2  = alloc((size_t)NB * NM * 2);
+  u16* WtH = (u16*)alloc((size_t)5 * ND * ND / 2);
+  u16* WtL = (u16*)alloc((size_t)5 * ND * ND / 2);
+  u16* keyH_t = (u16*)alloc((size_t)NB * NM * ND / 2);
+  u16* keyL_t = (u16*)alloc((size_t)NB * NM * ND / 2);
+  u16* keyH_s = (u16*)alloc((size_t)NB * NM * ND / 2);
+  u16* keyL_s = (u16*)alloc((size_t)NB * NM * ND / 2);
+  u16* valH_t = (u16*)alloc((size_t)NB * NNV * ND / 2);
+  u16* valL_t = (u16*)alloc((size_t)NB * NNV * ND / 2);
+  u16* valH_s = (u16*)alloc((size_t)NB * NM * ND / 2);
+  u16* valL_s = (u16*)alloc((size_t)NB * NM * ND / 2);
+  (void)ws_size; (void)in_sizes; (void)n_in; (void)out_size;
+
+  u16* tmpH = (u16*)kt_t;
+  u16* tmpL = (u16*)(kt_t + 1474560);
 
   float* out_type   = (float*)d_out;
   float* out_multi  = out_type + (size_t)NB * NM * NNV * 3;
@@ -774,13 +659,15 @@
 
   dim3 blk(256);
 
+  k_cvtT<<<dim3(15, 15, 5), blk, 0, stream>>>(bt_W, bi_W, WtH, WtL);
+
   Proj6 P;
-  P.c[0] = { key,   w_kt, b_kt, kt_t, NB * NM,  0, NM,  NM * NH };
-  P.c[1] = { value, w_vt, b_vt, vt_t, NB * NNV, 0, NNV, NNV * NH };
-  P.c[2] = { key,   w_ks, b_ks, kt_s, NB * NM,  0, NM,  NM * NH };
-  P.c[3] = { value, w_vs, b_vs, vt_s, NB * NM,  1, NM,  NNV * NH };
-  P.c[4] = { key,   w_km, b_km, kmf,  NB * NM,  0, NM,  NM * NH };
-  P.c[5] = { value, w_vm, b_vm, vmf,  NB * NM,  1, NM,  NNV * NH };
+  P.c[0] = { key,   w_kt, b_kt, kt_t, keyH_t, keyL_t, NB * NM,  0, NM,  NM * NH };
+  P.c[1] = { value, w_vt, b_vt, vt_t, valH_t, valL_t, NB * NNV, 0, NNV, NNV * NH };
+  P.c[2] = { key,   w_ks, b_ks, kt_s, keyH_s, keyL_s, NB * NM,  0, NM,  NM * NH };
+  P.c[3] = { value, w_vs, b_vs, vt_s, valH_s, valL_s, NB * NM,  1, NM,  NNV * NH };
+  P.c[4] = { key,   w_km, b_km, kmf,  nullptr, nullptr, NB * NM, 0, NM, NM * NH };
+  P.c[5] = { value, w_vm, b_vm, vmf,  nullptr, nullptr, NB * NM, 1, NM, NNV * NH };
   k_projM<<<dim3(193 * 10), blk, 0, stream>>>(P, NH);
 
   FoldCfg ft = { w_ffnt, b_ffnt, qkvt_w, qkvt_b, fold_t, 3 };
@@ -799,13 +686,16 @@
 
   k_multi<<<dim3((NB * NM * NM * 2 + 255) / 256), blk, 0, stream>>>(a2, b2, b_cls, out_multi);
 
-  run_rounds<3, NNV>(stream, kt_t, vt_t, key_mask, value_mask, 0, NNV,
-                     bt_W, bt_lw, bt_lb, fold_t, linK_t, linV_t,
-                     tmp, Y1, Y2, out_type);
+  k_mega<3, NNV><<<dim3(NB), dim3(1024), 0, stream>>>(
+      WtH, WtL, tmpH, tmpL, keyH_t, keyL_t, valH_t, valL_t,
+      key_mask, value_mask, 0, NNV,
+      fold_t, bt_lw, bt_lb, linK_t, linV_t, out_type);
 
   k_type<<<dim3(8), blk, 0, stream>>>(out_type, key_mask, km2);
 
-  run_rounds<2, NM>(stream, kt_s, vt_s, km2, value_mask, 1, NNV,
-                    bi_W, bi_lw, bi_lb, fold_s, linK_s, linV_s,
-                    tmp, Y1, Y2, out_single);
-}
+  k_mega<2, NM><<<dim3(NB), dim3(1024), 0, stream>>>(
+      WtH + (size_t)3 * ND * ND, WtL + (size_t)3 * ND * ND,
+      tmpH, tmpL, keyH_s, keyL_s, valH_s, valL_s,
+      km2, value_mask, 1, NNV,
+      fold_s, bi_lw, bi_lb, linK_s, linV_s, out_single);
+}
```

New measurement: 4.170 ms. 3.8x slower.
